# Kernel tuning notes

Hardware: AMD Instinct MI355X
Metric: run time of the kernel (lower is better)

The kernel has to match this reference:

```python
import jax, jax.numpy as jnp
import numpy as np

N_HEADS = 16
LATENT = 16          # latent_vec_len (1D RoPE portion of head_dim)
ROPE_BASE = 10000.0
HIDDEN = 1024


def _rope_1d_tables(seq_len, d):
    m = d // 2
    inv_freq = 1.0 / (ROPE_BASE ** (jnp.arange(m, dtype=jnp.float32) * 2.0 / d))
    ang = jnp.arange(seq_len, dtype=jnp.float32)[:, None] * inv_freq[None, :]  # (S, m)
    return jnp.cos(ang), jnp.sin(ang)


def _rope_2d_tables(height, width, d):
    m = d // 4
    inv_freq = 1.0 / (ROPE_BASE ** (jnp.arange(m, dtype=jnp.float32) * 4.0 / d))
    xa = jnp.arange(width, dtype=jnp.float32)[:, None] * inv_freq[None, :]   # (W, m)
    ya = jnp.arange(height, dtype=jnp.float32)[:, None] * inv_freq[None, :]  # (H, m)
    S = height * width
    cos_x = jnp.broadcast_to(jnp.cos(xa)[None, :, :], (height, width, m)).reshape(S, m)
    sin_x = jnp.broadcast_to(jnp.sin(xa)[None, :, :], (height, width, m)).reshape(S, m)
    cos_y = jnp.broadcast_to(jnp.cos(ya)[:, None, :], (height, width, m)).reshape(S, m)
    sin_y = jnp.broadcast_to(jnp.sin(ya)[:, None, :], (height, width, m)).reshape(S, m)
    return cos_x, sin_x, cos_y, sin_y


def _apply_rope_1d(x, cos, sin):
    # x: (B, n, S, d) with d even; cos/sin: (S, d//2)
    d = x.shape[-1]
    xr = x.reshape(*x.shape[:-1], d // 2, 2)
    a, b = xr[..., 0], xr[..., 1]
    na = a * cos - b * sin
    nb = a * sin + b * cos
    return jnp.stack((na, nb), axis=-1).reshape(x.shape)


def _apply_rope_2d(x, cos_x, sin_x, cos_y, sin_y):
    # x: (B, n, S, d) with d % 4 == 0; tables: (S, d//4)
    q = x.shape[-1] // 4
    xr, xi = x[..., :q], x[..., q:2 * q]
    yr, yi = x[..., 2 * q:3 * q], x[..., 3 * q:]
    return jnp.concatenate([
        xr * cos_x - xi * sin_x,
        xr * sin_x + xi * cos_x,
        yr * cos_y - yi * sin_y,
        yr * sin_y + yi * cos_y,
    ], axis=-1)


def setup_inputs() -> dict:
    key = jax.random.key(0)
    ks = jax.random.split(key, 9)
    B, S, D = 16, 1024, HIDDEN
    s = 1.0 / np.sqrt(D)
    inp = {
        'x': jax.random.normal(ks[0], (B, S, D), dtype=jnp.float32),
        'Wq': jax.random.uniform(ks[1], (D, D), jnp.float32, -s, s),
        'bq': jax.random.uniform(ks[2], (D,), jnp.float32, -s, s),
        'Wk': jax.random.uniform(ks[3], (D, D), jnp.float32, -s, s),
        'bk': jax.random.uniform(ks[4], (D,), jnp.float32, -s, s),
        'Wv': jax.random.uniform(ks[5], (D, D), jnp.float32, -s, s),
        'bv': jax.random.uniform(ks[6], (D,), jnp.float32, -s, s),
        'Wo': jax.random.uniform(ks[7], (D, D), jnp.float32, -s, s),
        'bo': jax.random.uniform(ks[8], (D,), jnp.float32, -s, s),
        'height': 32,
        'width': 32,
    }
    return inp


def reference(x, Wq, bq, Wk, bk, Wv, bv, Wo, bo, height, width):
    B, S, D = x.shape
    n, h = N_HEADS, D // N_HEADS
    spatial = h - LATENT
    scale = 1.0 / np.sqrt(h)

    def heads(t):
        return t.reshape(B, S, n, h).transpose(0, 2, 1, 3)  # (B, n, S, h)

    q = heads(x @ Wq.T + bq)
    k = heads(x @ Wk.T + bk)
    v = heads(x @ Wv.T + bv)

    cos1, sin1 = _rope_1d_tables(S, LATENT)
    cx, sx, cy, sy = _rope_2d_tables(height, width, spatial)

    ql = _apply_rope_1d(q[..., :LATENT], cos1, sin1)
    kl = _apply_rope_1d(k[..., :LATENT], cos1, sin1)
    qs = _apply_rope_2d(q[..., LATENT:], cx, sx, cy, sy)
    ks_ = _apply_rope_2d(k[..., LATENT:], cx, sx, cy, sy)

    qr = jnp.concatenate([ql, qs], axis=-1)
    kr = jnp.concatenate([kl, ks_], axis=-1)

    attn = jax.nn.softmax(jnp.einsum('bnsh,bnth->bnst', qr, kr) * scale, axis=-1)
    out = jnp.einsum('bnst,bnth->bnsh', attn, v)
    out = out.transpose(0, 2, 1, 3).reshape(B, S, D)
    return out @ Wo.T + bo
```

## Files before the change

kernel.cpp:

```cpp
#include <hip/hip_runtime.h>
#include <math.h>

#define B_ 16
#define S_ 1024
#define D_ 1024
#define NH_ 16
#define M_TOT (B_ * S_)

typedef __attribute__((ext_vector_type(8))) short short8v;
typedef __attribute__((ext_vector_type(4))) short short4v;
typedef __attribute__((ext_vector_type(4))) float float4v;
typedef __attribute__((ext_vector_type(4))) unsigned int uint4v;

static __device__ __forceinline__ unsigned short f2bf(float f) {
  union { float f; unsigned u; } x; x.f = f;
  unsigned r = (x.u + 0x7fffu + ((x.u >> 16) & 1u)) >> 16;
  return (unsigned short)r;
}
static __device__ __forceinline__ float bf2f(unsigned short u) {
  union { unsigned u; float f; } x; x.u = ((unsigned)u) << 16;
  return x.f;
}

static __device__ __forceinline__ unsigned pack2bf(float a, float b) {
  return ((unsigned)f2bf(b) << 16) | (unsigned)f2bf(a);
}

static __device__ __forceinline__ unsigned cvt_pk_bf16(float a, float b) {
  unsigned r;
  asm("v_cvt_pk_bf16_f32 %0, %1, %2" : "=v"(r) : "v"(a), "v"(b));
  return r;
}

static __device__ __forceinline__ void load_lds16(const unsigned short* g, unsigned short* l) {
  __builtin_amdgcn_global_load_lds(
      (const __attribute__((address_space(1))) unsigned int*)g,
      (__attribute__((address_space(3))) unsigned int*)l, 16, 0, 0);
}

__global__ __launch_bounds__(256) void prep(
    const float* __restrict__ x, unsigned short* __restrict__ xb,
    const float* __restrict__ w0, const float* __restrict__ w1,
    const float* __restrict__ w2, const float* __restrict__ w3,
    unsigned short* __restrict__ wdst,
    float* __restrict__ cos1, float* __restrict__ sin1,
    float* __restrict__ cos2, float* __restrict__ sin2) {
  const int bid = blockIdx.x;
  if (bid < 16384) {
    int i = bid * 256 + threadIdx.x;
    float4 v = ((const float4*)x)[i];
    unsigned short tt[4] = {f2bf(v.x), f2bf(v.y), f2bf(v.z), f2bf(v.w)};
    ((short4v*)xb)[i] = *(short4v*)tt;
  } else if (bid < 20480) {
    int wi = (bid - 16384) * 256 + threadIdx.x;
    int m = wi >> 18;
    int i = wi & 262143;
    const float* src = (m == 0) ? w0 : (m == 1) ? w1 : (m == 2) ? w2 : w3;
    float4 v = ((const float4*)src)[i];
    unsigned short tt[4] = {f2bf(v.x), f2bf(v.y), f2bf(v.z), f2bf(v.w)};
    ((short4v*)(wdst + (size_t)m * D_ * D_))[i] = *(short4v*)tt;
  } else {
    int t = (bid - 20480) * 256 + threadIdx.x;
    if (t < S_ * 8) {
      int s = t >> 3, i = t & 7;
      double ang = (double)s * pow(10000.0, -(double)i / 8.0);
      cos1[t] = (float)cos(ang);
      sin1[t] = (float)sin(ang);
    } else if (t < S_ * 8 + 384) {
      int u = t - S_ * 8;
      int p = u / 12, j = u - p * 12;
      double ang = (double)p * pow(10000.0, -(double)j / 12.0);
      cos2[u] = (float)cos(ang);
      sin2[u] = (float)sin(ang);
    }
  }
}

template <bool BF16OUT>
__global__ __launch_bounds__(256) void gemm_mfma(
    const unsigned short* __restrict__ A, const unsigned short* __restrict__ Wall,
    const float* __restrict__ b0, const float* __restrict__ b1,
    const float* __restrict__ b2, void* __restrict__ Cout) {
  __shared__ unsigned short As[3][128 * 32];
  __shared__ unsigned short Bs[3][128 * 32];
  const int y = blockIdx.y;
  const unsigned short* W = Wall + (size_t)y * D_ * D_;
  const float* bias = (y == 0) ? b0 : (y == 1) ? b1 : b2;
  const int t = threadIdx.x;
  const int w = t >> 6, L = t & 63;
  const int c = L & 15, g = L >> 4;
  const int id = blockIdx.x;
  const int xcd = id & 7, slot = id >> 3;
  const int bn = (slot & 7) * 128;
  const int bm = ((slot >> 3) * 8 + xcd) * 128;

  const int srow = w * 32 + (L >> 2);
  const int sko = (L & 3) * 8;
  const unsigned short* gA = A + (size_t)(bm + srow) * D_ + sko;
  const unsigned short* gB = W + (size_t)(bn + srow) * D_ + sko;

  const int wm = (w >> 1) * 64, wn = (w & 1) * 64;

  float4v acc[4][4];
#pragma unroll
  for (int i = 0; i < 4; ++i)
#pragma unroll
    for (int j = 0; j < 4; ++j) acc[i][j] = (float4v){0.f, 0.f, 0.f, 0.f};

#define GS(buf, kt_)                                                   \
  {                                                                    \
    load_lds16(gA + (kt_) * 32, &As[buf][w * 1024]);                   \
    load_lds16(gA + (kt_) * 32 + 16 * D_, &As[buf][w * 1024 + 512]);   \
    load_lds16(gB + (kt_) * 32, &Bs[buf][w * 1024]);                   \
    load_lds16(gB + (kt_) * 32 + 16 * D_, &Bs[buf][w * 1024 + 512]);   \
  }
#define VWAIT4 asm volatile("s_waitcnt vmcnt(4)" ::: "memory")
#define VWAIT0 asm volatile("s_waitcnt vmcnt(0)" ::: "memory")
#define BARRIER asm volatile("s_barrier" ::: "memory")
#define COMPUTE(cur)                                                     \
  {                                                                      \
    short8v af[4], bf[4];                                                \
    _Pragma("unroll")                                                    \
    for (int i = 0; i < 4; ++i)                                          \
      af[i] = *(const short8v*)&As[cur][(wm + 16 * i + c) * 32 + 8 * g]; \
    _Pragma("unroll")                                                    \
    for (int j = 0; j < 4; ++j)                                          \
      bf[j] = *(const short8v*)&Bs[cur][(wn + 16 * j + c) * 32 + 8 * g]; \
    _Pragma("unroll")                                                    \
    for (int i = 0; i < 4; ++i)                                          \
      _Pragma("unroll")                                                  \
      for (int j = 0; j < 4; ++j)                                        \
        acc[i][j] = __builtin_amdgcn_mfma_f32_16x16x32_bf16(             \
            af[i], bf[j], acc[i][j], 0, 0, 0);                           \
  }

  GS(0, 0);
  GS(1, 1);
#pragma unroll 1
  for (int s = 0; s < 30; s += 3) {
    VWAIT4; BARRIER; GS(2, s + 2); COMPUTE(0);
    VWAIT4; BARRIER; GS(0, s + 3); COMPUTE(1);
    VWAIT4; BARRIER; GS(1, s + 4); COMPUTE(2);
  }
  VWAIT4; BARRIER; COMPUTE(0);
  VWAIT0; BARRIER; COMPUTE(1);
#undef GS
#undef VWAIT4
#undef VWAIT0
#undef BARRIER
#undef COMPUTE
  unsigned short* Cb = (unsigned short*)Cout + (size_t)y * M_TOT * D_;
#pragma unroll
  for (int i = 0; i < 4; ++i)
#pragma unroll
    for (int r = 0; r < 4; ++r) {
      const size_t row = (size_t)bm + wm + 16 * i + 4 * g + r;
#pragma unroll
      for (int j = 0; j < 4; ++j) {
        const int col = bn + wn + 16 * j + c;
        float vv = acc[i][j][r] + bias[col];
        if (BF16OUT)
          Cb[row * D_ + col] = f2bf(vv);
        else
          ((float*)Cout)[row * D_ + col] = vv;
      }
    }
}

__global__ __launch_bounds__(256) void postproc(
    unsigned short* __restrict__ qb, unsigned short* __restrict__ kbuf,
    const unsigned short* __restrict__ vb, unsigned short* __restrict__ vT,
    const float* __restrict__ cos1, const float* __restrict__ sin1,
    const float* __restrict__ cos2, const float* __restrict__ sin2) {
  __shared__ unsigned short T[64][72];
  const int bid = blockIdx.x;
  if (bid < 2048) {
    const int qk = bid >> 10;
    unsigned short* buf = qk ? kbuf : qb;
    const float scale = qk ? 1.0f : 0.125f;
    const int tid = ((bid & 1023) << 8) + threadIdx.x;
    const int m = tid >> 4, head = tid & 15;
    const int s = m & (S_ - 1);
    const int xx = s & 31, yy = s >> 5;
    unsigned short* p = buf + (size_t)m * D_ + head * 64;

    unsigned short e[64];
#pragma unroll
    for (int v = 0; v < 8; ++v)
      *(short8v*)&e[8 * v] = *(const short8v*)(p + 8 * v);

    float c1v[8], s1v[8], cxv[12], sxv[12], cyv[12], syv[12];
#pragma unroll
    for (int i = 0; i < 8; ++i) {
      c1v[i] = cos1[s * 8 + i]; s1v[i] = sin1[s * 8 + i];
    }
#pragma unroll
    for (int j = 0; j < 12; ++j) {
      cxv[j] = cos2[xx * 12 + j]; sxv[j] = sin2[xx * 12 + j];
      cyv[j] = cos2[yy * 12 + j]; syv[j] = sin2[yy * 12 + j];
    }
#pragma unroll
    for (int i = 0; i < 8; ++i) {
      float a = bf2f(e[2 * i]), b = bf2f(e[2 * i + 1]);
      e[2 * i]     = f2bf((a * c1v[i] - b * s1v[i]) * scale);
      e[2 * i + 1] = f2bf((a * s1v[i] + b * c1v[i]) * scale);
    }
#pragma unroll
    for (int j = 0; j < 12; ++j) {
      float a = bf2f(e[16 + j]), b = bf2f(e[28 + j]);
      e[16 + j] = f2bf((a * cxv[j] - b * sxv[j]) * scale);
      e[28 + j] = f2bf((a * sxv[j] + b * cxv[j]) * scale);
      float a2 = bf2f(e[40 + j]), b2 = bf2f(e[52 + j]);
      e[40 + j] = f2bf((a2 * cyv[j] - b2 * syv[j]) * scale);
      e[52 + j] = f2bf((a2 * syv[j] + b2 * cyv[j]) * scale);
    }
#pragma unroll
    for (int v = 0; v < 8; ++v)
      *(short8v*)(p + 8 * v) = *(short8v*)&e[8 * v];
  } else {
    const int tb = bid - 2048;
    const int t = threadIdx.x;
    const int st0 = (tb & 15) * 64;
    const int hd = (tb >> 4) & 15, b = tb >> 8;
    const unsigned short* src = vb + ((size_t)b * S_ + st0) * D_ + hd * 64;
#pragma unroll
    for (int rep = 0; rep < 4; ++rep) {
      int id = t + rep * 256;
      int s = id >> 4, n4 = (id & 15) * 4;
      short4v val = *(const short4v*)(src + (size_t)s * D_ + n4);
      T[n4 + 0][s] = val[0]; T[n4 + 1][s] = val[1];
      T[n4 + 2][s] = val[2]; T[n4 + 3][s] = val[3];
    }
    __syncthreads();
    unsigned short* dst = vT + ((size_t)(b * NH_ + hd) * 64) * S_ + st0;
#pragma unroll
    for (int rep = 0; rep < 2; ++rep) {
      int id = t + rep * 256;
      int n = id >> 3, s8 = (id & 7) * 8;
      unsigned short tmp[8];
#pragma unroll
      for (int u2 = 0; u2 < 8; ++u2) tmp[u2] = T[n][s8 + u2];
      *(short8v*)(dst + (size_t)n * S_ + s8) = *(short8v*)tmp;
    }
  }
}

__global__ __launch_bounds__(256, 4) void attn_mfma(
    const unsigned short* __restrict__ qb, const unsigned short* __restrict__ kb,
    const unsigned short* __restrict__ vT, unsigned short* __restrict__ out) {
  __shared__ unsigned short KV[2][2][4096];
  const int t = threadIdx.x;
  const int w = t >> 6;
  const int L = t & 63;
  const int c = L & 15;
  const int g = L >> 4;
  const int id = blockIdx.x;
  const int xcd = id & 7, slot = id >> 3;
  const int qt = slot & 7;
  const int pair = (slot >> 3) * 8 + xcd;
  const int b = pair >> 4, hd = pair & 15;
  const size_t mrow0 = (size_t)b * S_ + qt * 128 + w * 32;
  const int dcol0 = hd * 64;

  const int lrow = L >> 3;
  const int lcol = ((L & 7) ^ lrow) * 8;

  const int a_lo = (((L & 16) ? 32 : 0) + c) * 4;
  const int a_hi = a_lo + 64;
  const bool ghi = (L >= 32);
  const int swz = (c & 7) << 3;

  short8v aq[2][2];
#pragma unroll
  for (int i = 0; i < 2; ++i)
#pragma unroll
    for (int st = 0; st < 2; ++st)
      aq[i][st] = *(const short8v*)(qb + (mrow0 + 16 * i + c) * D_ + dcol0 + 32 * st + 8 * g);

  float4v oacc[2][4];
  float lsum[2] = {0.f, 0.f};
#pragma unroll
  for (int i = 0; i < 2; ++i)
#pragma unroll
    for (int jv = 0; jv < 4; ++jv) oacc[i][jv] = (float4v){0.f, 0.f, 0.f, 0.f};

  const unsigned short* vbase = vT + (size_t)(b * NH_ + hd) * 64 * S_;
  const unsigned short* kbb = kb + (size_t)b * S_ * D_ + dcol0;

#define STAGE(buf, kt_)                                                          \
  {                                                                              \
    _Pragma("unroll")                                                            \
    for (int e = 0; e < 2; ++e) {                                                \
      const int seg = 2 * w + e;                                                 \
      const int row = seg * 8 + lrow;                                            \
      load_lds16(kbb + (size_t)((kt_) * 64 + row) * D_ + lcol,                   \
                 &KV[buf][0][seg * 512]);                                        \
      load_lds16(vbase + (size_t)row * S_ + (kt_) * 64 + lcol,                   \
                 &KV[buf][1][seg * 512]);                                        \
    }                                                                            \
  }

  STAGE(0, 0);
  asm volatile("s_waitcnt vmcnt(0)" ::: "memory");
  __syncthreads();

#pragma unroll 1
  for (int kt = 0; kt < 16; ++kt) {
    const int cur = kt & 1;
    if (kt < 15) STAGE(cur ^ 1, kt + 1);
#pragma unroll
    for (int st = 0; st < 2; ++st) {
      short8v vfh[4];
#pragma unroll
      for (int jv = 0; jv < 4; ++jv)
        vfh[jv] = *(const short8v*)&KV[cur][1][((16 * jv + c) * 64 + st * 32 + 8 * g) ^ swz];
      short8v kfh[2][2];
#pragma unroll
      for (int jl = 0; jl < 2; ++jl)
#pragma unroll
        for (int h = 0; h < 2; ++h)
          kfh[jl][h] = *(const short8v*)&KV[cur][0][((16 * (2 * st + jl) + c) * 64 + h * 32 + 8 * g) ^ swz];
      float4v sacch[2][2];
#pragma unroll
      for (int i = 0; i < 2; ++i)
#pragma unroll
        for (int jl = 0; jl < 2; ++jl) sacch[i][jl] = (float4v){0.f, 0.f, 0.f, 0.f};
      __builtin_amdgcn_s_setprio(1);
#pragma unroll
      for (int jl = 0; jl < 2; ++jl)
#pragma unroll
        for (int i = 0; i < 2; ++i) {
          sacch[i][jl] = __builtin_amdgcn_mfma_f32_16x16x32_bf16(kfh[jl][0], aq[i][0], sacch[i][jl], 0, 0, 0);
          sacch[i][jl] = __builtin_amdgcn_mfma_f32_16x16x32_bf16(kfh[jl][1], aq[i][1], sacch[i][jl], 0, 0, 0);
        }
      __builtin_amdgcn_s_setprio(0);
      unsigned pkh[2][2][2];
#pragma unroll
      for (int i = 0; i < 2; ++i)
#pragma unroll
        for (int jl = 0; jl < 2; ++jl) {
          float p0 = __expf(sacch[i][jl][0]);
          float p1 = __expf(sacch[i][jl][1]);
          float p2 = __expf(sacch[i][jl][2]);
          float p3 = __expf(sacch[i][jl][3]);
          const unsigned w0 = cvt_pk_bf16(p0, p1);
          const unsigned w1 = cvt_pk_bf16(p2, p3);
          pkh[i][jl][0] = w0;
          pkh[i][jl][1] = w1;
          union { unsigned u; float f; } t0, t1, t2, t3;
          t0.u = w0 << 16; t1.u = w0 & 0xffff0000u;
          t2.u = w1 << 16; t3.u = w1 & 0xffff0000u;
          lsum[i] += (t0.f + t1.f) + (t2.f + t3.f);
        }
      short8v aph[2];
#pragma unroll
      for (int i = 0; i < 2; ++i) {
        uint4v wv;
#pragma unroll
        for (int q2 = 0; q2 < 4; ++q2) {
          const int addr = (q2 & 2) ? a_hi : a_lo;
          int vlo = __builtin_amdgcn_ds_bpermute(addr, (int)pkh[i][0][q2 & 1]);
          int vhi = __builtin_amdgcn_ds_bpermute(addr, (int)pkh[i][1][q2 & 1]);
          wv[q2] = (unsigned)(ghi ? vhi : vlo);
        }
        aph[i] = *(short8v*)&wv;
      }
      __builtin_amdgcn_s_setprio(1);
#pragma unroll
      for (int jv = 0; jv < 4; ++jv)
#pragma unroll
        for (int i = 0; i < 2; ++i)
          oacc[i][jv] = __builtin_amdgcn_mfma_f32_16x16x32_bf16(aph[i], vfh[jv], oacc[i][jv], 0, 0, 0);
      __builtin_amdgcn_s_setprio(0);
    }
    asm volatile("s_waitcnt vmcnt(0)" ::: "memory");
    __syncthreads();
  }
#undef STAGE
#pragma unroll
  for (int i = 0; i < 2; ++i) {
    float ls = lsum[i];
    ls += __shfl_xor(ls, 16);
    ls += __shfl_xor(ls, 32);
#pragma unroll
    for (int r = 0; r < 4; ++r) {
      float inv = 1.f / __shfl(ls, 4 * g + r);
      size_t row = mrow0 + 16 * i + 4 * g + r;
#pragma unroll
      for (int jv = 0; jv < 4; ++jv)
        out[row * D_ + dcol0 + 16 * jv + c] = f2bf(oacc[i][jv][r] * inv);
    }
  }
}

extern "C" void kernel_launch(void* const* d_in, const int* in_sizes, int n_in,
                              void* d_out, int out_size, void* d_ws, size_t ws_size,
                              hipStream_t stream) {
  const float* x  = (const float*)d_in[0];
  const float* Wq = (const float*)d_in[1];
  const float* bq = (const float*)d_in[2];
  const float* Wk = (const float*)d_in[3];
  const float* bk = (const float*)d_in[4];
  const float* Wv = (const float*)d_in[5];
  const float* bv = (const float*)d_in[6];
  const float* Wo = (const float*)d_in[7];
  const float* bo = (const float*)d_in[8];
  float* out = (float*)d_out;

  char* ws = (char*)d_ws;
  const size_t SZ2 = (size_t)M_TOT * D_ * 2;
  unsigned short* xb = (unsigned short*)(ws);
  unsigned short* ob = xb;
  unsigned short* qb = (unsigned short*)(ws + SZ2);
  unsigned short* kb = (unsigned short*)(ws + 2 * SZ2);
  unsigned short* vb = (unsigned short*)(ws + 3 * SZ2);
  unsigned short* vT = (unsigned short*)(ws + 4 * SZ2);
  unsigned short* wqb = (unsigned short*)(ws + 5 * SZ2);
  unsigned short* wob = wqb + 3 * (size_t)D_ * D_;
  float* cos1 = (float*)(ws + 5 * SZ2 + 4 * (size_t)D_ * D_ * 2);
  float* sin1 = cos1 + S_ * 8;
  float* cos2 = sin1 + S_ * 8;
  float* sin2 = cos2 + 384;

  prep<<<20514, 256, 0, stream>>>(x, xb, Wq, Wk, Wv, Wo, wqb,
                                  cos1, sin1, cos2, sin2);
  gemm_mfma<true><<<dim3(1024, 3), 256, 0, stream>>>(xb, wqb, bq, bk, bv, qb);
  postproc<<<6144, 256, 0, stream>>>(qb, kb, vb, vT, cos1, sin1, cos2, sin2);
  attn_mfma<<<2048, 256, 0, stream>>>(qb, kb, vT, ob);
  gemm_mfma<false><<<dim3(1024, 1), 256, 0, stream>>>(ob, wob, bo, bo, bo, out);
}
```

Measured before the change: 457.6 us.

## Widen GEMM block tile to 128x256 with eight waves per block

```diff
diff --git a/kernel.cpp b/kernel.cpp
--- a/kernel.cpp
+++ b/kernel.cpp
@@ -20,10 +20,6 @@
 static __device__ __forceinline__ float bf2f(unsigned short u) {
   union { unsigned u; float f; } x; x.u = ((unsigned)u) << 16;
   return x.f;
-}
-
-static __device__ __forceinline__ unsigned pack2bf(float a, float b) {
-  return ((unsigned)f2bf(b) << 16) | (unsigned)f2bf(a);
 }
 
 static __device__ __forceinline__ unsigned cvt_pk_bf16(float a, float b) {
@@ -77,29 +73,27 @@
 }
 
 template <bool BF16OUT>
-__global__ __launch_bounds__(256) void gemm_mfma(
+__global__ __launch_bounds__(512, 4) void gemm_mfma(
     const unsigned short* __restrict__ A, const unsigned short* __restrict__ Wall,
     const float* __restrict__ b0, const float* __restrict__ b1,
     const float* __restrict__ b2, void* __restrict__ Cout) {
   __shared__ unsigned short As[3][128 * 32];
-  __shared__ unsigned short Bs[3][128 * 32];
+  __shared__ unsigned short Bs[3][256 * 32];
   const int y = blockIdx.y;
   const unsigned short* W = Wall + (size_t)y * D_ * D_;
   const float* bias = (y == 0) ? b0 : (y == 1) ? b1 : b2;
   const int t = threadIdx.x;
-  const int w = t >> 6, L = t & 63;
+  const int wid = t >> 6, L = t & 63;
   const int c = L & 15, g = L >> 4;
   const int id = blockIdx.x;
   const int xcd = id & 7, slot = id >> 3;
-  const int bn = (slot & 7) * 128;
-  const int bm = ((slot >> 3) * 8 + xcd) * 128;
-
-  const int srow = w * 32 + (L >> 2);
-  const int sko = (L & 3) * 8;
-  const unsigned short* gA = A + (size_t)(bm + srow) * D_ + sko;
-  const unsigned short* gB = W + (size_t)(bn + srow) * D_ + sko;
-
-  const int wm = (w >> 1) * 64, wn = (w & 1) * 64;
+  const int bn = (slot & 3) * 256;
+  const int bm = ((slot >> 2) * 8 + xcd) * 128;
+
+  const unsigned short* gA = A + (size_t)(bm + (t >> 2)) * D_ + (t & 3) * 8;
+  const unsigned short* gB = W + (size_t)(bn + (t >> 2)) * D_ + (t & 3) * 8;
+
+  const int wm = (wid >> 2) * 64, wn = (wid & 3) * 64;
 
   float4v acc[4][4];
 #pragma unroll
@@ -107,14 +101,13 @@
 #pragma unroll
     for (int j = 0; j < 4; ++j) acc[i][j] = (float4v){0.f, 0.f, 0.f, 0.f};
 
-#define GS(buf, kt_)                                                   \
-  {                                                                    \
-    load_lds16(gA + (kt_) * 32, &As[buf][w * 1024]);                   \
-    load_lds16(gA + (kt_) * 32 + 16 * D_, &As[buf][w * 1024 + 512]);   \
-    load_lds16(gB + (kt_) * 32, &Bs[buf][w * 1024]);                   \
-    load_lds16(gB + (kt_) * 32 + 16 * D_, &Bs[buf][w * 1024 + 512]);   \
-  }
-#define VWAIT4 asm volatile("s_waitcnt vmcnt(4)" ::: "memory")
+#define GS(buf, kt_)                                                     \
+  {                                                                      \
+    load_lds16(gA + (kt_) * 32, &As[buf][wid * 512]);                    \
+    load_lds16(gB + (kt_) * 32, &Bs[buf][wid * 512]);                    \
+    load_lds16(gB + (kt_) * 32 + 128 * D_, &Bs[buf][wid * 512 + 4096]);  \
+  }
+#define VWAIT3 asm volatile("s_waitcnt vmcnt(3)" ::: "memory")
 #define VWAIT0 asm volatile("s_waitcnt vmcnt(0)" ::: "memory")
 #define BARRIER asm volatile("s_barrier" ::: "memory")
 #define COMPUTE(cur)                                                     \
@@ -138,14 +131,14 @@
   GS(1, 1);
 #pragma unroll 1
   for (int s = 0; s < 30; s += 3) {
-    VWAIT4; BARRIER; GS(2, s + 2); COMPUTE(0);
-    VWAIT4; BARRIER; GS(0, s + 3); COMPUTE(1);
-    VWAIT4; BARRIER; GS(1, s + 4); COMPUTE(2);
-  }
-  VWAIT4; BARRIER; COMPUTE(0);
+    VWAIT3; BARRIER; GS(2, s + 2); COMPUTE(0);
+    VWAIT3; BARRIER; GS(0, s + 3); COMPUTE(1);
+    VWAIT3; BARRIER; GS(1, s + 4); COMPUTE(2);
+  }
+  VWAIT3; BARRIER; COMPUTE(0);
   VWAIT0; BARRIER; COMPUTE(1);
 #undef GS
-#undef VWAIT4
+#undef VWAIT3
 #undef VWAIT0
 #undef BARRIER
 #undef COMPUTE
@@ -424,8 +417,8 @@
 
   prep<<<20514, 256, 0, stream>>>(x, xb, Wq, Wk, Wv, Wo, wqb,
                                   cos1, sin1, cos2, sin2);
-  gemm_mfma<true><<<dim3(1024, 3), 256, 0, stream>>>(xb, wqb, bq, bk, bv, qb);
+  gemm_mfma<true><<<dim3(512, 3), 512, 0, stream>>>(xb, wqb, bq, bk, bv, qb);
   postproc<<<6144, 256, 0, stream>>>(qb, kb, vb, vT, cos1, sin1, cos2, sin2);
   attn_mfma<<<2048, 256, 0, stream>>>(qb, kb, vT, ob);
-  gemm_mfma<false><<<dim3(1024, 1), 256, 0, stream>>>(ob, wob, bo, bo, bo, out);
-}
+  gemm_mfma<false><<<dim3(512, 1), 512, 0, stream>>>(ob, wob, bo, bo, bo, out);
+}
```

After: 426.5 us. 6.8% less time.
